# Optimization experiments

Measured on AMD Instinct MI355X. Metric: run time of the kernel, lower is better.

The kernel has to match this reference:

```python
import jax, jax.numpy as jnp
import numpy as np

D = 256   # input_dim (also per-head dim)
H = 8     # num_heads
B = 32
S = 1024


def setup_inputs() -> dict:
    key = jax.random.key(0)
    ks = jax.random.split(key, 9)
    scale = 1.0 / np.sqrt(D)
    x = jax.random.normal(ks[0], (B, S, D), dtype=jnp.float32)
    Wk = jax.random.normal(ks[1], (D, D * H), dtype=jnp.float32) * scale
    bk = jnp.zeros((D * H,), dtype=jnp.float32)
    Wv = jax.random.normal(ks[2], (D, D * H), dtype=jnp.float32) * scale
    bv = jnp.zeros((D * H,), dtype=jnp.float32)
    query = jax.random.normal(ks[3], (H, D), dtype=jnp.float32)
    Wo = jax.random.normal(ks[4], (D * H, D), dtype=jnp.float32) / np.sqrt(D * H)
    bo = jnp.zeros((D,), dtype=jnp.float32)
    return {"x": x, "Wk": Wk, "bk": bk, "Wv": Wv, "bv": bv,
            "query": query, "Wo": Wo, "bo": bo}


def reference(x, Wk, bk, Wv, bv, query, Wo, bo):
    b, s, _ = x.shape
    # keys/values: [B, S, H, D]
    keys = (x @ Wk + bk).reshape(b, s, H, D)
    values = (x @ Wv + bv).reshape(b, s, H, D)
    # per-head single-query scores over sequence: [B, S, H]
    scores = jnp.einsum("bshd,hd->bsh", keys, query)
    attn = jax.nn.softmax(scores, axis=1)
    # attention-pooled values per head: [B, H, D] -> concat [B, H*D]
    pooled = jnp.einsum("bsh,bshd->bhd", attn, values).reshape(b, H * D)
    return pooled @ Wo + bo
```

## Files before the change

kernel.cpp:

```cpp
#include <hip/hip_runtime.h>

#define D 256
#define H 8
#define B 32
#define S 1024
#define SCH 32
#define SCS 32

#define OFF_QK     0
#define OFF_SB     2048
#define OFF_ML     2056
#define OFF_XWP    18440
#define OFF_POOLED 2115592

__global__ void k_prep(const float* __restrict__ Wk, const float* __restrict__ bk,
                       const float* __restrict__ query, const float* __restrict__ bo,
                       float* __restrict__ qk, float* __restrict__ sb,
                       float* __restrict__ out) {
    __shared__ float red[256];
    const int h  = blockIdx.x >> 5;
    const int kc = blockIdx.x & 31;
    const int t  = threadIdx.x;
    const int kl = t >> 5;
    const int dq = t & 31;
    const int k  = kc * 8 + kl;
    const int d0 = dq * 8;
    const float* wrow = Wk + (size_t)k * (D * H) + h * D + d0;
    const float* qrow = query + h * D + d0;
    const float4 w0 = *(const float4*)(wrow);
    const float4 w1 = *(const float4*)(wrow + 4);
    const float4 q0 = *(const float4*)(qrow);
    const float4 q1 = *(const float4*)(qrow + 4);
    float acc = w0.x * q0.x + w0.y * q0.y + w0.z * q0.z + w0.w * q0.w
              + w1.x * q1.x + w1.y * q1.y + w1.z * q1.z + w1.w * q1.w;
    #pragma unroll
    for (int msk = 1; msk < 32; msk <<= 1) acc += __shfl_xor(acc, msk);
    if (dq == 0) qk[h * D + k] = acc;
    if (kc == 0) {
        red[t] = bk[h * D + t] * query[h * D + t];
        __syncthreads();
        for (int st = 128; st > 0; st >>= 1) {
            if (t < st) red[t] += red[t + st];
            __syncthreads();
        }
        if (t == 0) sb[h] = red[0];
    }
    if (h == 0) out[(size_t)kc * D + t] = bo[t];
}

__global__ void k_fused(const float* __restrict__ x, const float* __restrict__ qk,
                        const float* __restrict__ sb, float* __restrict__ xwp,
                        float2* __restrict__ mlbuf) {
    const int b  = blockIdx.x >> 5;
    const int c  = blockIdx.x & 31;
    const int s0 = c * SCS;
    const int t  = threadIdx.x;
    __shared__ float qkL[H * D];
    __shared__ float sbL[H];
    __shared__ float sc[SCS][H];
    {
        float4* q4 = (float4*)qkL;
        q4[t]       = ((const float4*)qk)[t];
        q4[t + 256] = ((const float4*)qk)[t + 256];
        if (t < H) sbL[t] = sb[t];
    }
    __syncthreads();

    {
        const int sl = t >> 3;
        const int dq = t & 7;
        const int d0 = dq * 32;
        const float* xrow = x + ((size_t)(b * S + s0 + sl)) * D + d0;
        float4 xr[8];
        #pragma unroll
        for (int j0 = 0; j0 < 8; j0++) {
            const int j = (j0 + dq) & 7;
            xr[j0] = *(const float4*)(xrow + j * 4);
        }
        float accA[H] = {};
        #pragma unroll
        for (int j0 = 0; j0 < 8; j0++) {
            const int j = (j0 + dq) & 7;
            const float4 xv = xr[j0];
            #pragma unroll
            for (int hh = 0; hh < H; hh++) {
                const float4 qv = *(const float4*)(&qkL[hh * D + d0 + j * 4]);
                accA[hh] += xv.x * qv.x + xv.y * qv.y + xv.z * qv.z + xv.w * qv.w;
            }
        }
        #pragma unroll
        for (int hh = 0; hh < H; hh++) {
            accA[hh] += __shfl_xor(accA[hh], 1);
            accA[hh] += __shfl_xor(accA[hh], 2);
            accA[hh] += __shfl_xor(accA[hh], 4);
        }
        if (dq == 0) {
            #pragma unroll
            for (int hh = 0; hh < H; hh++)
                sc[sl][hh] = accA[hh] + sbL[hh];
        }
    }
    __syncthreads();

    {
        const int hh = t >> 5;
        const int u  = t & 31;
        const float v = sc[u][hh];
        float m = v;
        #pragma unroll
        for (int msk = 1; msk < 32; msk <<= 1) m = fmaxf(m, __shfl_xor(m, msk));
        const float e = __expf(v - m);
        float sum = e;
        #pragma unroll
        for (int msk = 1; msk < 32; msk <<= 1) sum += __shfl_xor(sum, msk);
        sc[u][hh] = e;
        if (u == 0) mlbuf[((size_t)(b * SCH + c)) * H + hh] = make_float2(m, sum);
    }
    __syncthreads();

    {
        float acc2[H] = {};
        const float* xp = x + ((size_t)(b * S + s0)) * D + t;
        #pragma unroll 4
        for (int s = 0; s < SCS; s++) {
            const float xv = xp[(size_t)s * D];
            const float4 pa = *(const float4*)(&sc[s][0]);
            const float4 pb = *(const float4*)(&sc[s][4]);
            acc2[0] += pa.x * xv; acc2[1] += pa.y * xv;
            acc2[2] += pa.z * xv; acc2[3] += pa.w * xv;
            acc2[4] += pb.x * xv; acc2[5] += pb.y * xv;
            acc2[6] += pb.z * xv; acc2[7] += pb.w * xv;
        }
        #pragma unroll
        for (int hh = 0; hh < H; hh++)
            xwp[(((size_t)(b * SCH + c)) * H + hh) * D + t] = acc2[hh];
    }
}

__global__ void k_pooled(const float* __restrict__ xwp, const float2* __restrict__ mlbuf,
                         const float* __restrict__ Wv, const float* __restrict__ bv,
                         float* __restrict__ pooled) {
    const int bh = blockIdx.x;
    const int b = bh >> 3, h = bh & 7;
    const int j = threadIdx.x;
    __shared__ float xwL[D];
    __shared__ float scaleL[SCH];
    __shared__ float2 mlL[SCH];
    if (j < SCH) mlL[j] = mlbuf[((size_t)(b * SCH + j)) * H + h];
    __syncthreads();
    if (j == 0) {
        float M = -1e30f;
        for (int cc = 0; cc < SCH; cc++) M = fmaxf(M, mlL[cc].x);
        float L = 0.f;
        for (int cc = 0; cc < SCH; cc++) L += mlL[cc].y * __expf(mlL[cc].x - M);
        const float invL = 1.f / L;
        for (int cc = 0; cc < SCH; cc++) scaleL[cc] = __expf(mlL[cc].x - M) * invL;
    }
    __syncthreads();
    float acc = 0.f;
    #pragma unroll
    for (int cc = 0; cc < SCH; cc++)
        acc += xwp[(((size_t)(b * SCH + cc)) * H + h) * D + j] * scaleL[cc];
    xwL[j] = acc;
    __syncthreads();
    const float* wcol = Wv + h * D + j;
    float a2 = 0.f;
    #pragma unroll 8
    for (int d = 0; d < D; d++)
        a2 += xwL[d] * wcol[(size_t)d * (D * H)];
    pooled[(size_t)b * (D * H) + h * D + j] = a2 + bv[h * D + j];
}

__global__ void k_out(const float* __restrict__ pooled, const float* __restrict__ Wo,
                      float* __restrict__ out) {
    const int b  = blockIdx.x >> 3;
    const int kc = blockIdx.x & 7;
    const int j  = threadIdx.x;
    __shared__ float pL[256];
    pL[j] = pooled[(size_t)b * (D * H) + kc * 256 + j];
    __syncthreads();
    const float* wp = Wo + (size_t)(kc * 256) * D + j;
    float acc = 0.f;
    #pragma unroll 8
    for (int cc = 0; cc < 256; cc++)
        acc += pL[cc] * wp[(size_t)cc * D];
    atomicAdd(out + (size_t)b * D + j, acc);
}

extern "C" void kernel_launch(void* const* d_in, const int* in_sizes, int n_in,
                              void* d_out, int out_size, void* d_ws, size_t ws_size,
                              hipStream_t stream) {
    const float* x     = (const float*)d_in[0];
    const float* Wk    = (const float*)d_in[1];
    const float* bk    = (const float*)d_in[2];
    const float* Wv    = (const float*)d_in[3];
    const float* bv    = (const float*)d_in[4];
    const float* query = (const float*)d_in[5];
    const float* Wo    = (const float*)d_in[6];
    const float* bo    = (const float*)d_in[7];
    float* out = (float*)d_out;
    float* ws  = (float*)d_ws;

    float*  qk     = ws + OFF_QK;
    float*  sb     = ws + OFF_SB;
    float2* mlbuf  = (float2*)(ws + OFF_ML);
    float*  xwp    = ws + OFF_XWP;
    float*  pooled = ws + OFF_POOLED;

    k_prep<<<dim3(H * 32), dim3(256), 0, stream>>>(Wk, bk, query, bo, qk, sb, out);
    k_fused<<<dim3(B * SCH), dim3(256), 0, stream>>>(x, qk, sb, xwp, mlbuf);
    k_pooled<<<dim3(B * H), dim3(256), 0, stream>>>(xwp, mlbuf, Wv, bv, pooled);
    k_out<<<dim3(B * 8), dim3(256), 0, stream>>>(pooled, Wo, out);
}
```

Baseline: 128.6 us.

## Halve sequence chunk count and split pooled/out GEMVs across more blocks with atomics

The fused scoring kernel now processes 64-row sequence chunks, using 16 chunks per batch instead of 32. Each row is handled by four threads instead of eight, and x is loaded inline rather than prefetched into registers. This halves the partial-sum buffer that k_pooled must reduce. k_pooled and k_out each split their reduction dimension in two and combine the halves with atomicAdd, doubling the block count; the pooled output is pre-initialised with bv in k_prep. The extra parallelism targets the small-grid GEMV stages, at the cost of more atomics and less parallelism in the fused stage.

```diff
diff --git a/kernel.cpp b/kernel.cpp
--- a/kernel.cpp
+++ b/kernel.cpp
@@ -4,19 +4,21 @@
 #define H 8
 #define B 32
 #define S 1024
-#define SCH 32
-#define SCS 32
+#define SCH 16
+#define SCS 64
 
 #define OFF_QK     0
 #define OFF_SB     2048
 #define OFF_ML     2056
-#define OFF_XWP    18440
-#define OFF_POOLED 2115592
-
-__global__ void k_prep(const float* __restrict__ Wk, const float* __restrict__ bk,
-                       const float* __restrict__ query, const float* __restrict__ bo,
-                       float* __restrict__ qk, float* __restrict__ sb,
-                       float* __restrict__ out) {
+#define OFF_XWP    10248
+#define OFF_POOLED 1058824
+
+__global__ void __launch_bounds__(256) k_prep(
+        const float* __restrict__ Wk, const float* __restrict__ bk,
+        const float* __restrict__ query, const float* __restrict__ bo,
+        const float* __restrict__ bv,
+        float* __restrict__ qk, float* __restrict__ sb,
+        float* __restrict__ out, float* __restrict__ pooled) {
     __shared__ float red[256];
     const int h  = blockIdx.x >> 5;
     const int kc = blockIdx.x & 31;
@@ -45,14 +47,16 @@
         }
         if (t == 0) sb[h] = red[0];
     }
+    pooled[(size_t)kc * (D * H) + h * D + t] = bv[h * D + t];
     if (h == 0) out[(size_t)kc * D + t] = bo[t];
 }
 
-__global__ void k_fused(const float* __restrict__ x, const float* __restrict__ qk,
-                        const float* __restrict__ sb, float* __restrict__ xwp,
-                        float2* __restrict__ mlbuf) {
-    const int b  = blockIdx.x >> 5;
-    const int c  = blockIdx.x & 31;
+__global__ void __launch_bounds__(256) k_fused(
+        const float* __restrict__ x, const float* __restrict__ qk,
+        const float* __restrict__ sb, float* __restrict__ xwp,
+        float2* __restrict__ mlbuf) {
+    const int b  = blockIdx.x >> 4;
+    const int c  = blockIdx.x & 15;
     const int s0 = c * SCS;
     const int t  = threadIdx.x;
     __shared__ float qkL[H * D];
@@ -67,21 +71,15 @@
     __syncthreads();
 
     {
-        const int sl = t >> 3;
-        const int dq = t & 7;
-        const int d0 = dq * 32;
+        const int sl = t >> 2;
+        const int dq = t & 3;
+        const int d0 = dq * 64;
         const float* xrow = x + ((size_t)(b * S + s0 + sl)) * D + d0;
-        float4 xr[8];
-        #pragma unroll
-        for (int j0 = 0; j0 < 8; j0++) {
-            const int j = (j0 + dq) & 7;
-            xr[j0] = *(const float4*)(xrow + j * 4);
-        }
         float accA[H] = {};
         #pragma unroll
-        for (int j0 = 0; j0 < 8; j0++) {
-            const int j = (j0 + dq) & 7;
-            const float4 xv = xr[j0];
+        for (int j0 = 0; j0 < 16; j0++) {
+            const int j = (j0 + dq * 4) & 15;
+            const float4 xv = *(const float4*)(xrow + j * 4);
             #pragma unroll
             for (int hh = 0; hh < H; hh++) {
                 const float4 qv = *(const float4*)(&qkL[hh * D + d0 + j * 4]);
@@ -92,7 +90,6 @@
         for (int hh = 0; hh < H; hh++) {
             accA[hh] += __shfl_xor(accA[hh], 1);
             accA[hh] += __shfl_xor(accA[hh], 2);
-            accA[hh] += __shfl_xor(accA[hh], 4);
         }
         if (dq == 0) {
             #pragma unroll
@@ -105,15 +102,16 @@
     {
         const int hh = t >> 5;
         const int u  = t & 31;
-        const float v = sc[u][hh];
-        float m = v;
+        const float v0 = sc[u][hh], v1 = sc[u + 32][hh];
+        float m = fmaxf(v0, v1);
         #pragma unroll
         for (int msk = 1; msk < 32; msk <<= 1) m = fmaxf(m, __shfl_xor(m, msk));
-        const float e = __expf(v - m);
-        float sum = e;
+        const float e0 = __expf(v0 - m), e1 = __expf(v1 - m);
+        float sum = e0 + e1;
         #pragma unroll
         for (int msk = 1; msk < 32; msk <<= 1) sum += __shfl_xor(sum, msk);
-        sc[u][hh] = e;
+        sc[u][hh] = e0;
+        sc[u + 32][hh] = e1;
         if (u == 0) mlbuf[((size_t)(b * SCH + c)) * H + hh] = make_float2(m, sum);
     }
     __syncthreads();
@@ -137,13 +135,15 @@
     }
 }
 
-__global__ void k_pooled(const float* __restrict__ xwp, const float2* __restrict__ mlbuf,
-                         const float* __restrict__ Wv, const float* __restrict__ bv,
-                         float* __restrict__ pooled) {
-    const int bh = blockIdx.x;
+__global__ void __launch_bounds__(256) k_pooled(
+        const float* __restrict__ xwp, const float2* __restrict__ mlbuf,
+        const float* __restrict__ Wv, float* __restrict__ pooled) {
+    const int blk = blockIdx.x;
+    const int bh  = blk >> 1;
+    const int dh  = blk & 1;
     const int b = bh >> 3, h = bh & 7;
     const int j = threadIdx.x;
-    __shared__ float xwL[D];
+    __shared__ float xwL[D / 2];
     __shared__ float scaleL[SCH];
     __shared__ float2 mlL[SCH];
     if (j < SCH) mlL[j] = mlbuf[((size_t)(b * SCH + j)) * H + h];
@@ -157,32 +157,36 @@
         for (int cc = 0; cc < SCH; cc++) scaleL[cc] = __expf(mlL[cc].x - M) * invL;
     }
     __syncthreads();
-    float acc = 0.f;
-    #pragma unroll
-    for (int cc = 0; cc < SCH; cc++)
-        acc += xwp[(((size_t)(b * SCH + cc)) * H + h) * D + j] * scaleL[cc];
-    xwL[j] = acc;
-    __syncthreads();
-    const float* wcol = Wv + h * D + j;
+    if (j < D / 2) {
+        const int d = dh * (D / 2) + j;
+        float acc = 0.f;
+        #pragma unroll
+        for (int cc = 0; cc < SCH; cc++)
+            acc += xwp[(((size_t)(b * SCH + cc)) * H + h) * D + d] * scaleL[cc];
+        xwL[j] = acc;
+    }
+    __syncthreads();
+    const float* wcol = Wv + (size_t)(dh * (D / 2)) * (D * H) + h * D + j;
     float a2 = 0.f;
     #pragma unroll 8
-    for (int d = 0; d < D; d++)
+    for (int d = 0; d < D / 2; d++)
         a2 += xwL[d] * wcol[(size_t)d * (D * H)];
-    pooled[(size_t)b * (D * H) + h * D + j] = a2 + bv[h * D + j];
-}
-
-__global__ void k_out(const float* __restrict__ pooled, const float* __restrict__ Wo,
-                      float* __restrict__ out) {
-    const int b  = blockIdx.x >> 3;
-    const int kc = blockIdx.x & 7;
+    atomicAdd(pooled + (size_t)b * (D * H) + h * D + j, a2);
+}
+
+__global__ void __launch_bounds__(256) k_out(
+        const float* __restrict__ pooled, const float* __restrict__ Wo,
+        float* __restrict__ out) {
+    const int b  = blockIdx.x >> 4;
+    const int kc = blockIdx.x & 15;
     const int j  = threadIdx.x;
-    __shared__ float pL[256];
-    pL[j] = pooled[(size_t)b * (D * H) + kc * 256 + j];
-    __syncthreads();
-    const float* wp = Wo + (size_t)(kc * 256) * D + j;
+    __shared__ float pL[128];
+    if (j < 128) pL[j] = pooled[(size_t)b * (D * H) + kc * 128 + j];
+    __syncthreads();
+    const float* wp = Wo + (size_t)(kc * 128) * D + j;
     float acc = 0.f;
     #pragma unroll 8
-    for (int cc = 0; cc < 256; cc++)
+    for (int cc = 0; cc < 128; cc++)
         acc += pL[cc] * wp[(size_t)cc * D];
     atomicAdd(out + (size_t)b * D + j, acc);
 }
@@ -207,8 +211,8 @@
     float*  xwp    = ws + OFF_XWP;
     float*  pooled = ws + OFF_POOLED;
 
-    k_prep<<<dim3(H * 32), dim3(256), 0, stream>>>(Wk, bk, query, bo, qk, sb, out);
+    k_prep<<<dim3(H * 32), dim3(256), 0, stream>>>(Wk, bk, query, bo, bv, qk, sb, out, pooled);
     k_fused<<<dim3(B * SCH), dim3(256), 0, stream>>>(x, qk, sb, xwp, mlbuf);
-    k_pooled<<<dim3(B * H), dim3(256), 0, stream>>>(xwp, mlbuf, Wv, bv, pooled);
-    k_out<<<dim3(B * 8), dim3(256), 0, stream>>>(pooled, Wo, out);
-}
+    k_pooled<<<dim3(B * H * 2), dim3(256), 0, stream>>>(xwp, mlbuf, Wv, pooled);
+    k_out<<<dim3(B * 16), dim3(256), 0, stream>>>(pooled, Wo, out);
+}
```

Result: faster. 115.1 us (-10.5%).
